# Performance work log

Hardware: AMD Instinct MI355X
Metric: run time of the kernel (lower is better)

Reference implementation:

```python
import jax, jax.numpy as jnp
import numpy as np

B, S, D = 2, 1024, 1024
H, KV, HD = 16, 4, 64
E, F = 8, 3584
EPS = 1e-5
TOP_K = 2


def setup_inputs() -> dict:
    key = jax.random.key(0)
    ks = jax.random.split(key, 12)
    sc = 0.02
    inv_freq = 1.0 / (10000.0 ** (np.arange(0, HD, 2, dtype=np.float32) / HD))
    freqs = np.outer(np.arange(S, dtype=np.float32), inv_freq)
    emb = np.concatenate([freqs, freqs], axis=-1)  # [S, HD]
    return {
        'x': jax.random.normal(ks[0], (B, S, D), jnp.float32),
        'ln1_w': jnp.ones((D,), jnp.float32),
        'ln2_w': jnp.ones((D,), jnp.float32),
        'wq': jax.random.normal(ks[1], (H * HD, D), jnp.float32) * sc,
        'wk': jax.random.normal(ks[2], (KV * HD, D), jnp.float32) * sc,
        'wv': jax.random.normal(ks[3], (KV * HD, D), jnp.float32) * sc,
        'wo': jax.random.normal(ks[4], (D, H * HD), jnp.float32) * sc,
        'gate_w': jax.random.normal(ks[5], (E, D), jnp.float32) * sc,
        'w1': jax.random.normal(ks[6], (E, F, D), jnp.float32) * sc,
        'w2': jax.random.normal(ks[7], (E, D, F), jnp.float32) * sc,
        'w3': jax.random.normal(ks[8], (E, F, D), jnp.float32) * sc,
        'cos': jnp.asarray(np.cos(emb)),
        'sin': jnp.asarray(np.sin(emb)),
    }


def _rms_norm(x, w):
    var = jnp.mean(jnp.square(x), axis=-1, keepdims=True)
    return x * jax.lax.rsqrt(var + EPS) * w


def _rotate_half(x):
    x1, x2 = jnp.split(x, 2, axis=-1)
    return jnp.concatenate([-x2, x1], axis=-1)


def _attn(h, wq, wk, wv, wo, cos, sin):
    # h: [B,S,D]
    q = (h @ wq.T).reshape(B, S, H, HD).transpose(0, 2, 1, 3)      # [B,H,S,HD]
    k = (h @ wk.T).reshape(B, S, KV, HD).transpose(0, 2, 1, 3)     # [B,KV,S,HD]
    v = (h @ wv.T).reshape(B, S, KV, HD).transpose(0, 2, 1, 3)
    c = cos[None, None, :S, :]
    s = sin[None, None, :S, :]
    q = q * c + _rotate_half(q) * s
    k = k * c + _rotate_half(k) * s
    k = jnp.repeat(k, H // KV, axis=1)  # GQA expand -> [B,H,S,HD]
    v = jnp.repeat(v, H // KV, axis=1)
    scores = jnp.einsum('bhqd,bhkd->bhqk', q, k) / jnp.sqrt(jnp.float32(HD))
    causal = jnp.tril(jnp.ones((S, S), bool))
    scores = jnp.where(causal[None, None], scores, jnp.float32(-1e30))
    probs = jax.nn.softmax(scores, axis=-1)
    out = jnp.einsum('bhqk,bhkd->bhqd', probs, v)
    out = out.transpose(0, 2, 1, 3).reshape(B, S, H * HD)
    return out @ wo.T


def _moe(h, gate_w, w1, w2, w3):
    T = B * S
    hs = h.reshape(T, D)
    probs = jax.nn.softmax(hs @ gate_w.T, axis=-1)       # [T,E]
    _, sel = jax.lax.top_k(probs, TOP_K)                  # [T,2]
    rw = jnp.take_along_axis(probs, sel, axis=-1)
    rw = rw / jnp.sum(rw, axis=-1, keepdims=True)
    cw = jnp.zeros((T, E), hs.dtype).at[jnp.arange(T)[:, None], sel].add(rw)  # [T,E] combine weights
    h1 = jnp.einsum('td,efd->tef', hs, w1)               # [T,E,F]
    h3 = jnp.einsum('td,efd->tef', hs, w3)
    inter = jax.nn.silu(h1) * h3
    out = jnp.einsum('tef,edf,te->td', inter, w2, cw)
    return out.reshape(B, S, D)


def reference(x, ln1_w, ln2_w, wq, wk, wv, wo, gate_w, w1, w2, w3, cos, sin):
    h = x + _attn(_rms_norm(x, ln1_w), wq, wk, wv, wo, cos, sin)
    h = h + _moe(_rms_norm(h, ln2_w), gate_w, w1, w2, w3)
    return h
```

## Files before the change

### kernel.cpp

```cpp
#include <hip/hip_runtime.h>

typedef unsigned short u16;
using short8 = __attribute__((ext_vector_type(8))) short;
using f32x4  = __attribute__((ext_vector_type(4))) float;

#define TQ   2048
#define DM   1024
#define SLEN 1024
#define FDIM 3584
#define NEXP 8

static __device__ __forceinline__ u16 f2bf(float f) {
  union { float f; unsigned u; } a; a.f = f;
  unsigned r = a.u + 0x7fffu + ((a.u >> 16) & 1u);
  return (u16)(r >> 16);
}
static __device__ __forceinline__ float bf2f(u16 u) {
  union { unsigned u; float f; } a; a.u = ((unsigned)u) << 16;
  return a.f;
}
static __device__ __forceinline__ unsigned cvtpk(float lo, float hi) {
  unsigned r;
  asm volatile("v_cvt_pk_bf16_f32 %0, %1, %2" : "=v"(r) : "v"(lo), "v"(hi));
  return r;
}

static __device__ __forceinline__ void gload16(const void* g, void* l) {
  __builtin_amdgcn_global_load_lds((const __attribute__((address_space(1))) void*)g,
                                   (__attribute__((address_space(3))) void*)l, 16, 0, 0);
}

static __device__ __forceinline__ int xcd_lid(int bid, int cpx) {
  return (bid & 7) * cpx + (bid >> 3);
}

static __device__ __forceinline__ void cvtwr8(float4 a, float4 b, u16* dst) {
  uint4 u;
  u.x = cvtpk(a.x, a.y); u.y = cvtpk(a.z, a.w);
  u.z = cvtpk(b.x, b.y); u.w = cvtpk(b.z, b.w);
  *(uint4*)dst = u;
}

__global__ __launch_bounds__(256) void fused_pre_kernel(
    const float* __restrict__ x, const float* __restrict__ ln1,
    u16* __restrict__ oh, u16* __restrict__ ol,
    const float* __restrict__ wq, const float* __restrict__ wk,
    const float* __restrict__ wv, const float* __restrict__ wo,
    u16* __restrict__ qkvh, u16* __restrict__ qkvl,
    u16* __restrict__ woh, u16* __restrict__ wol) {
  int tid = threadIdx.x;
  if (blockIdx.x < 2048) {
    int t = blockIdx.x;
    const float4* xr = (const float4*)(x + (size_t)t * DM);
    float4 v = xr[tid];
    float ss = v.x * v.x + v.y * v.y + v.z * v.z + v.w * v.w;
#pragma unroll
    for (int m = 1; m < 64; m <<= 1) ss += __shfl_xor(ss, m);
    __shared__ float red[4];
    if ((tid & 63) == 0) red[tid >> 6] = ss;
    __syncthreads();
    float tot = red[0] + red[1] + red[2] + red[3];
    float sc = rsqrtf(tot * (1.0f / DM) + 1e-5f);
    float4 wv_ = ((const float4*)ln1)[tid];
    float o0 = v.x * sc * wv_.x, o1 = v.y * sc * wv_.y;
    float o2 = v.z * sc * wv_.z, o3 = v.w * sc * wv_.w;
    ushort4 hh;
    hh.x = f2bf(o0); hh.y = f2bf(o1); hh.z = f2bf(o2); hh.w = f2bf(o3);
    *(ushort4*)(oh + (size_t)t * DM + tid * 4) = hh;
    ushort4 ll;
    ll.x = f2bf(o0 - bf2f(hh.x)); ll.y = f2bf(o1 - bf2f(hh.y));
    ll.z = f2bf(o2 - bf2f(hh.z)); ll.w = f2bf(o3 - bf2f(hh.w));
    *(ushort4*)(ol + (size_t)t * DM + tid * 4) = ll;
    return;
  }
  int wb = blockIdx.x - 2048;
  for (int i = wb * 256 + tid; i < 655360; i += 640 * 256) {
    int el = i * 4;
    const float* src; u16 *dh, *dl;
    if (el < 1572864) {
      int r = el >> 10, c = el & 1023;
      if (r < 1024) src = wq + el;
      else if (r < 1280) src = wk + (r - 1024) * 1024 + c;
      else src = wv + (r - 1280) * 1024 + c;
      dh = qkvh + el; dl = qkvl + el;
    } else {
      int e2 = el - 1572864;
      src = wo + e2; dh = woh + e2; dl = wol + e2;
    }
    float4 v = *(const float4*)src;
    ushort4 h, l;
    h.x = f2bf(v.x); h.y = f2bf(v.y); h.z = f2bf(v.z); h.w = f2bf(v.w);
    l.x = f2bf(v.x - bf2f(h.x)); l.y = f2bf(v.y - bf2f(h.y));
    l.z = f2bf(v.z - bf2f(h.z)); l.w = f2bf(v.w - bf2f(h.w));
    *(ushort4*)dh = h; *(ushort4*)dl = l;
  }
}

__global__ __launch_bounds__(256) void rmsnorm_gate_kernel(
    const float* __restrict__ x, const float* __restrict__ w,
    const float* __restrict__ gw, u16* __restrict__ oh,
    int* cnt, int* tok_e, int* tok_pos, float* tok_w) {
  int t = blockIdx.x, tid = threadIdx.x;
  float4 v = ((const float4*)(x + (size_t)t * DM))[tid];
  float ss = v.x * v.x + v.y * v.y + v.z * v.z + v.w * v.w;
#pragma unroll
  for (int m = 1; m < 64; m <<= 1) ss += __shfl_xor(ss, m);
  __shared__ float red[4];
  __shared__ float gred[4][8];
  if ((tid & 63) == 0) red[tid >> 6] = ss;
  __syncthreads();
  float tot = red[0] + red[1] + red[2] + red[3];
  float sc = rsqrtf(tot * (1.0f / DM) + 1e-5f);
  float4 wv_ = ((const float4*)w)[tid];
  float o0 = v.x * sc * wv_.x, o1 = v.y * sc * wv_.y;
  float o2 = v.z * sc * wv_.z, o3 = v.w * sc * wv_.w;
  ushort4 hh;
  hh.x = f2bf(o0); hh.y = f2bf(o1); hh.z = f2bf(o2); hh.w = f2bf(o3);
  *(ushort4*)(oh + (size_t)t * DM + tid * 4) = hh;
  float acc[8];
#pragma unroll
  for (int e = 0; e < 8; e++) {
    float4 ge = ((const float4*)(gw + e * DM))[tid];
    acc[e] = o0 * ge.x + o1 * ge.y + o2 * ge.z + o3 * ge.w;
  }
#pragma unroll
  for (int e = 0; e < 8; e++)
#pragma unroll
    for (int m = 1; m < 64; m <<= 1) acc[e] += __shfl_xor(acc[e], m);
  int lane = tid & 63, wvi = tid >> 6;
  if (lane == 0)
#pragma unroll
    for (int e = 0; e < 8; e++) gred[wvi][e] = acc[e];
  __syncthreads();
  if (tid == 0) {
    float l[8];
#pragma unroll
    for (int e = 0; e < 8; e++)
      l[e] = gred[0][e] + gred[1][e] + gred[2][e] + gred[3][e];
    int i0 = 0;
#pragma unroll
    for (int e = 1; e < 8; e++) if (l[e] > l[i0]) i0 = e;
    int i1 = -1;
#pragma unroll
    for (int e = 0; e < 8; e++) if (e != i0 && (i1 < 0 || l[e] > l[i1])) i1 = e;
    float w0 = 1.0f;
    float w1 = expf(l[i1] - l[i0]);
    float rs = 1.0f / (w0 + w1);
    int p0 = atomicAdd(&cnt[i0], 1);
    int p1 = atomicAdd(&cnt[i1], 1);
    tok_e[t * 2] = i0; tok_e[t * 2 + 1] = i1;
    tok_pos[t * 2] = p0; tok_pos[t * 2 + 1] = p1;
    tok_w[t * 2] = w0 * rs; tok_w[t * 2 + 1] = w1 * rs;
  }
}

__global__ __launch_bounds__(256) void qkv_rope_kernel(
    const u16* __restrict__ Ah, const u16* __restrict__ Al,
    const u16* __restrict__ Wh, const u16* __restrict__ Wl,
    const float* __restrict__ cosT, const float* __restrict__ sinT,
    u16* __restrict__ qh, u16* __restrict__ ql,
    u16* __restrict__ kh, u16* __restrict__ kl,
    u16* __restrict__ vh, u16* __restrict__ vl, int cpx) {
  __shared__ __align__(16) char pool[73728];
  u16 (*sAh)[128][32] = (u16(*)[128][32])pool;
  u16 (*sAl)[128][32] = (u16(*)[128][32])(pool + 24576);
  u16 (*sWh)[64][32]  = (u16(*)[64][32])(pool + 49152);
  u16 (*sWl)[64][32]  = (u16(*)[64][32])(pool + 61440);
  float (*sEpi)[65]   = (float(*)[65])pool;
  int lid = xcd_lid(blockIdx.x, cpx);
  int bm = lid & 15, bn = lid >> 4;
  int tid = threadIdx.x, lane = tid & 63, w = tid >> 6;
  int wm = w >> 1, wn = w & 1;
  int qi = lane & 15, g = lane >> 4;
  int lr = lane >> 2, lc = (lane & 3) * 8;
  const u16* pa0 = Ah + (size_t)(bm * 128 + w * 16 + lr) * DM + lc;
  const u16* pa1 = pa0 + 64 * DM;
  const u16* pl0 = Al + (size_t)(bm * 128 + w * 16 + lr) * DM + lc;
  const u16* pl1 = pl0 + 64 * DM;
  const u16* pw  = Wh + (size_t)(bn * 64 + w * 16 + lr) * DM + lc;
  const u16* pwl = Wl + (size_t)(bn * 64 + w * 16 + lr) * DM + lc;
  f32x4 acc[4][2] = {};
#define STGQ(buf, kk) do { \
    gload16(pa0 + (kk), &sAh[buf][w * 16][0]); \
    gload16(pa1 + (kk), &sAh[buf][64 + w * 16][0]); \
    gload16(pl0 + (kk), &sAl[buf][w * 16][0]); \
    gload16(pl1 + (kk), &sAl[buf][64 + w * 16][0]); \
    gload16(pw  + (kk), &sWh[buf][w * 16][0]); \
    gload16(pwl + (kk), &sWl[buf][w * 16][0]); } while (0)
  STGQ(0, 0);
  STGQ(1, 32);
  for (int ks = 0; ks < 32; ks++) {
    int cur = ks % 3;
    if (ks == 31) asm volatile("s_waitcnt vmcnt(0) lgkmcnt(0)" ::: "memory");
    else          asm volatile("s_waitcnt vmcnt(6) lgkmcnt(0)" ::: "memory");
    __builtin_amdgcn_s_barrier();
    short8 afh[4], afl[4], bfh[2], bfl[2];
#pragma unroll
    for (int i = 0; i < 4; i++) {
      afh[i] = *(short8*)&sAh[cur][wm * 64 + i * 16 + qi][g * 8];
      afl[i] = *(short8*)&sAl[cur][wm * 64 + i * 16 + qi][g * 8];
    }
#pragma unroll
    for (int i = 0; i < 2; i++) {
      bfh[i] = *(short8*)&sWh[cur][wn * 32 + i * 16 + qi][g * 8];
      bfl[i] = *(short8*)&sWl[cur][wn * 32 + i * 16 + qi][g * 8];
    }
    __builtin_amdgcn_s_setprio(1);
#pragma unroll
    for (int mi = 0; mi < 4; mi++)
#pragma unroll
      for (int ni = 0; ni < 2; ni++) {
        f32x4 a = acc[mi][ni];
        a = __builtin_amdgcn_mfma_f32_16x16x32_bf16(afh[mi], bfh[ni], a, 0, 0, 0);
        a = __builtin_amdgcn_mfma_f32_16x16x32_bf16(afl[mi], bfh[ni], a, 0, 0, 0);
        a = __builtin_amdgcn_mfma_f32_16x16x32_bf16(afh[mi], bfl[ni], a, 0, 0, 0);
        acc[mi][ni] = a;
      }
    __builtin_amdgcn_s_setprio(0);
    if (ks < 30) STGQ((ks + 2) % 3, (ks + 2) * 32);
  }
#undef STGQ
  __syncthreads();
#pragma unroll
  for (int mi = 0; mi < 4; mi++)
#pragma unroll
    for (int ni = 0; ni < 2; ni++)
#pragma unroll
      for (int r = 0; r < 4; r++)
        sEpi[wm * 64 + mi * 16 + g * 4 + r][wn * 32 + ni * 16 + qi] = acc[mi][ni][r];
  __syncthreads();
  int r0 = tid >> 1, hc = (tid & 1) * 16;
  int t = bm * 128 + r0;
  int s = t & (SLEN - 1);
  union { ushort u[16]; uint4 v[2]; } h1, l1, h2, l2;
  if (bn < 20) {
#pragma unroll
    for (int j = 0; j < 16; j++) {
      int d = hc + j;
      float c = cosT[s * 64 + d], sn = sinT[s * 64 + d];
      float x1 = sEpi[r0][d], x2 = sEpi[r0][d + 32];
      float o1 = x1 * c - x2 * sn;
      float o2 = x2 * c + x1 * sn;
      h1.u[j] = f2bf(o1); l1.u[j] = f2bf(o1 - bf2f(h1.u[j]));
      h2.u[j] = f2bf(o2); l2.u[j] = f2bf(o2 - bf2f(h2.u[j]));
    }
    u16 *dh, *dl; size_t base;
    if (bn < 16) { dh = qh; dl = ql; base = (size_t)t * DM + bn * 64; }
    else         { dh = kh; dl = kl; base = (size_t)t * 256 + (bn - 16) * 64; }
    *(uint4*)(dh + base + hc)      = h1.v[0];
    *(uint4*)(dh + base + hc + 8)  = h1.v[1];
    *(uint4*)(dh + base + 32 + hc)     = h2.v[0];
    *(uint4*)(dh + base + 32 + hc + 8) = h2.v[1];
    *(uint4*)(dl + base + hc)      = l1.v[0];
    *(uint4*)(dl + base + hc + 8)  = l1.v[1];
    *(uint4*)(dl + base + 32 + hc)     = l2.v[0];
    *(uint4*)(dl + base + 32 + hc + 8) = l2.v[1];
  } else {
#pragma unroll
    for (int j = 0; j < 16; j++) {
      float x1 = sEpi[r0][hc + j], x2 = sEpi[r0][hc + 32 + j];
      h1.u[j] = f2bf(x1); l1.u[j] = f2bf(x1 - bf2f(h1.u[j]));
      h2.u[j] = f2bf(x2); l2.u[j] = f2bf(x2 - bf2f(h2.u[j]));
    }
    size_t base = (size_t)t * 256 + (bn - 20) * 64;
    *(uint4*)(vh + base + hc)      = h1.v[0];
    *(uint4*)(vh + base + hc + 8)  = h1.v[1];
    *(uint4*)(vh + base + 32 + hc)     = h2.v[0];
    *(uint4*)(vh + base + 32 + hc + 8) = h2.v[1];
    *(uint4*)(vl + base + hc)      = l1.v[0];
    *(uint4*)(vl + base + hc + 8)  = l1.v[1];
    *(uint4*)(vl + base + 32 + hc)     = l2.v[0];
    *(uint4*)(vl + base + 32 + hc + 8) = l2.v[1];
  }
}

template <bool RESID>
__global__ __launch_bounds__(256) void gemm_split3_kernel(
    const u16* __restrict__ Ah, const u16* __restrict__ Al,
    const u16* __restrict__ Wh, const u16* __restrict__ Wl,
    float* __restrict__ C, const float* __restrict__ resid, int N, int cpx) {
  __shared__ u16 sAh[3][128][32], sAl[3][128][32], sWh[3][64][32], sWl[3][64][32];
  int lid = xcd_lid(blockIdx.x, cpx);
  int bm = lid & 15, bn = lid >> 4;
  int tid = threadIdx.x, lane = tid & 63, w = tid >> 6;
  int wm = w >> 1, wn = w & 1;
  int qi = lane & 15, g = lane >> 4;
  int lr = lane >> 2, lc = (lane & 3) * 8;
  const u16* pa0 = Ah + (size_t)(bm * 128 + w * 16 + lr) * DM + lc;
  const u16* pa1 = pa0 + 64 * DM;
  const u16* pl0 = Al + (size_t)(bm * 128 + w * 16 + lr) * DM + lc;
  const u16* pl1 = pl0 + 64 * DM;
  const u16* pw  = Wh + (size_t)(bn * 64 + w * 16 + lr) * DM + lc;
  const u16* pwl = Wl + (size_t)(bn * 64 + w * 16 + lr) * DM + lc;
  f32x4 acc[4][2] = {};
#define STG3(buf, kk) do { \
    gload16(pa0 + (kk), &sAh[buf][w * 16][0]); \
    gload16(pa1 + (kk), &sAh[buf][64 + w * 16][0]); \
    gload16(pl0 + (kk), &sAl[buf][w * 16][0]); \
    gload16(pl1 + (kk), &sAl[buf][64 + w * 16][0]); \
    gload16(pw  + (kk), &sWh[buf][w * 16][0]); \
    gload16(pwl + (kk), &sWl[buf][w * 16][0]); } while (0)
  STG3(0, 0);
  STG3(1, 32);
  for (int ks = 0; ks < 32; ks++) {
    int cur = ks % 3;
    if (ks == 31) asm volatile("s_waitcnt vmcnt(0) lgkmcnt(0)" ::: "memory");
    else          asm volatile("s_waitcnt vmcnt(6) lgkmcnt(0)" ::: "memory");
    __builtin_amdgcn_s_barrier();
    short8 afh[4], afl[4], bfh[2], bfl[2];
#pragma unroll
    for (int i = 0; i < 4; i++) {
      afh[i] = *(short8*)&sAh[cur][wm * 64 + i * 16 + qi][g * 8];
      afl[i] = *(short8*)&sAl[cur][wm * 64 + i * 16 + qi][g * 8];
    }
#pragma unroll
    for (int i = 0; i < 2; i++) {
      bfh[i] = *(short8*)&sWh[cur][wn * 32 + i * 16 + qi][g * 8];
      bfl[i] = *(short8*)&sWl[cur][wn * 32 + i * 16 + qi][g * 8];
    }
    __builtin_amdgcn_s_setprio(1);
#pragma unroll
    for (int mi = 0; mi < 4; mi++)
#pragma unroll
      for (int ni = 0; ni < 2; ni++) {
        f32x4 a = acc[mi][ni];
        a = __builtin_amdgcn_mfma_f32_16x16x32_bf16(afh[mi], bfh[ni], a, 0, 0, 0);
        a = __builtin_amdgcn_mfma_f32_16x16x32_bf16(afl[mi], bfh[ni], a, 0, 0, 0);
        a = __builtin_amdgcn_mfma_f32_16x16x32_bf16(afh[mi], bfl[ni], a, 0, 0, 0);
        acc[mi][ni] = a;
      }
    __builtin_amdgcn_s_setprio(0);
    if (ks < 30) STG3((ks + 2) % 3, (ks + 2) * 32);
  }
#undef STG3
#pragma unroll
  for (int mi = 0; mi < 4; mi++)
#pragma unroll
    for (int ni = 0; ni < 2; ni++) {
      int col = bn * 64 + wn * 32 + ni * 16 + qi;
#pragma unroll
      for (int r = 0; r < 4; r++) {
        int row = bm * 128 + wm * 64 + mi * 16 + g * 4 + r;
        float val = acc[mi][ni][r];
        if (RESID) val += resid[(size_t)row * N + col];
        C[(size_t)row * N + col] = val;
      }
    }
}

__global__ __launch_bounds__(256) void attn_kernel(
    const u16* __restrict__ qh, const u16* __restrict__ ql,
    const u16* __restrict__ kh, const u16* __restrict__ kl,
    const u16* __restrict__ vh, const u16* __restrict__ vl,
    u16* __restrict__ oh, u16* __restrict__ ol) {
  __shared__ u16 sKh[64][72], sKl[64][72];
  __shared__ u16 sVh[64][72], sVl[64][72];
  __shared__ u16 sPh[4][16][72], sPl[4][16][72];
  int idx = blockIdx.x & 255;
  int p = idx & 7;
  int bh = idx >> 3;
  int b = bh >> 4, h = bh & 15, kvh = h >> 2;
  int qt = (blockIdx.x < 256) ? p : (15 - p);
  int tid = threadIdx.x, lane = tid & 63, w = tid >> 6;
  int qi = lane & 15, g = lane >> 4;
  int qrow = qt * 64 + w * 16 + qi;
  size_t qbase = ((size_t)(b * SLEN + qrow)) * DM + h * 64;
  short8 qfh[2], qfl[2];
#pragma unroll
  for (int ds = 0; ds < 2; ds++) {
    qfh[ds] = *(const short8*)(qh + qbase + ds * 32 + g * 8);
    qfl[ds] = *(const short8*)(ql + qbase + ds * 32 + g * 8);
  }
  f32x4 oacc[4] = {};
  float mrun = -1e30f, lrun = 0.f;
  int ktiles = qt + 1;
  for (int kt = 0; kt < ktiles; kt++) {
    __syncthreads();
    {
      int r = tid >> 3, cs = (tid & 7) * 8;
#pragma unroll
      for (int rr = 0; rr < 64; rr += 32) {
        int key = kt * 64 + rr + r;
        size_t src = ((size_t)(b * SLEN + key)) * 256 + kvh * 64 + cs;
        *(short8*)&sKh[rr + r][cs] = *(const short8*)(kh + src);
        *(short8*)&sKl[rr + r][cs] = *(const short8*)(kl + src);
        short8 vv = *(const short8*)(vh + src);
        short8 vv2 = *(const short8*)(vl + src);
#pragma unroll
        for (int j = 0; j < 8; j++) {
          sVh[cs + j][rr + r] = (u16)vv[j];
          sVl[cs + j][rr + r] = (u16)vv2[j];
        }
      }
    }
    __syncthreads();
    f32x4 sa[4];
#pragma unroll
    for (int kf = 0; kf < 4; kf++) {
      f32x4 a = {};
#pragma unroll
      for (int ds = 0; ds < 2; ds++) {
        short8 kfh = *(short8*)&sKh[kf * 16 + qi][ds * 32 + g * 8];
        short8 kfl = *(short8*)&sKl[kf * 16 + qi][ds * 32 + g * 8];
        a = __builtin_amdgcn_mfma_f32_16x16x32_bf16(kfh, qfh[ds], a, 0, 0, 0);
        a = __builtin_amdgcn_mfma_f32_16x16x32_bf16(kfl, qfh[ds], a, 0, 0, 0);
        a = __builtin_amdgcn_mfma_f32_16x16x32_bf16(kfh, qfl[ds], a, 0, 0, 0);
      }
      sa[kf] = a;
    }
    int qg = qt * 64 + w * 16 + qi;
    float sv[4][4];
    float tmax = -1e30f;
#pragma unroll
    for (int kf = 0; kf < 4; kf++)
#pragma unroll
      for (int r = 0; r < 4; r++) {
        int key = kt * 64 + kf * 16 + g * 4 + r;
        float s = sa[kf][r] * 0.125f;
        s = (key <= qg) ? s : -1e30f;
        sv[kf][r] = s;
        tmax = fmaxf(tmax, s);
      }
    tmax = fmaxf(tmax, __shfl_xor(tmax, 16));
    tmax = fmaxf(tmax, __shfl_xor(tmax, 32));
    float mn = fmaxf(mrun, tmax);
    float alpha = expf(mrun - mn);
    float psum = 0.f;
#pragma unroll
    for (int kf = 0; kf < 4; kf++) {
      float p0 = expf(sv[kf][0] - mn), p1 = expf(sv[kf][1] - mn);
      float p2 = expf(sv[kf][2] - mn), p3 = expf(sv[kf][3] - mn);
      psum += p0 + p1 + p2 + p3;
      ushort4 ph, pl;
      ph.x = f2bf(p0); ph.y = f2bf(p1); ph.z = f2bf(p2); ph.w = f2bf(p3);
      pl.x = f2bf(p0 - bf2f(ph.x)); pl.y = f2bf(p1 - bf2f(ph.y));
      pl.z = f2bf(p2 - bf2f(ph.z)); pl.w = f2bf(p3 - bf2f(ph.w));
      *(ushort4*)&sPh[w][qi][kf * 16 + g * 4] = ph;
      *(ushort4*)&sPl[w][qi][kf * 16 + g * 4] = pl;
    }
    psum += __shfl_xor(psum, 16);
    psum += __shfl_xor(psum, 32);
    lrun = lrun * alpha + psum;
    mrun = mn;
#pragma unroll
    for (int df = 0; df < 4; df++) {
      oacc[df][0] *= alpha; oacc[df][1] *= alpha;
      oacc[df][2] *= alpha; oacc[df][3] *= alpha;
    }
#pragma unroll
    for (int ks = 0; ks < 2; ks++) {
      short8 pfh = *(short8*)&sPh[w][qi][ks * 32 + g * 8];
      short8 pfl = *(short8*)&sPl[w][qi][ks * 32 + g * 8];
#pragma unroll
      for (int df = 0; df < 4; df++) {
        short8 vfh = *(short8*)&sVh[df * 16 + qi][ks * 32 + g * 8];
        short8 vfl = *(short8*)&sVl[df * 16 + qi][ks * 32 + g * 8];
        f32x4 a = oacc[df];
        a = __builtin_amdgcn_mfma_f32_16x16x32_bf16(vfh, pfh, a, 0, 0, 0);
        a = __builtin_amdgcn_mfma_f32_16x16x32_bf16(vfl, pfh, a, 0, 0, 0);
        a = __builtin_amdgcn_mfma_f32_16x16x32_bf16(vfh, pfl, a, 0, 0, 0);
        oacc[df] = a;
      }
    }
  }
  float inv = 1.0f / lrun;
  size_t obase = ((size_t)(b * SLEN + qt * 64 + w * 16 + qi)) * DM + h * 64;
#pragma unroll
  for (int df = 0; df < 4; df++) {
    float o0 = oacc[df][0] * inv, o1 = oacc[df][1] * inv;
    float o2 = oacc[df][2] * inv, o3 = oacc[df][3] * inv;
    ushort4 hh, ll;
    hh.x = f2bf(o0); hh.y = f2bf(o1); hh.z = f2bf(o2); hh.w = f2bf(o3);
    ll.x = f2bf(o0 - bf2f(hh.x)); ll.y = f2bf(o1 - bf2f(hh.y));
    ll.z = f2bf(o2 - bf2f(hh.z)); ll.w = f2bf(o3 - bf2f(hh.w));
    *(ushort4*)(oh + obase + df * 16 + g * 4) = hh;
    *(ushort4*)(ol + obase + df * 16 + g * 4) = ll;
  }
}

__global__ void zero8_kernel(int* p) { if (threadIdx.x < 8) p[threadIdx.x] = 0; }

__global__ void schedule_kernel(const int* cnt, int* offs, int* mt,
                                int* row_e, int* row_bm) {
  if (threadIdx.x == 0) {
    int s = 0, m = 0;
    for (int e = 0; e < 8; e++) {
      offs[e] = s;
      int nb = (cnt[e] + 127) >> 7;
      for (int i = 0; i < nb; i++) { row_e[m] = e; row_bm[m] = i; m++; }
      s += cnt[e];
    }
    *mt = m;
  }
}

__global__ __launch_bounds__(256) void gather_kernel(
    const u16* __restrict__ hn2b, const int* __restrict__ tok_e,
    const int* __restrict__ tok_pos, const float* __restrict__ tok_w,
    const int* __restrict__ offs, u16* __restrict__ Xg,
    int* __restrict__ pair_tok, int* __restrict__ pair_slot, float* __restrict__ pair_w) {
  int t = blockIdx.x;
#pragma unroll
  for (int slot = 0; slot < 2; slot++) {
    int e = tok_e[t * 2 + slot];
    int p = offs[e] + tok_pos[t * 2 + slot];
    ((ushort4*)(Xg + (size_t)p * DM))[threadIdx.x] =
        ((const ushort4*)(hn2b + (size_t)t * DM))[threadIdx.x];
    if (threadIdx.x == 0) {
      pair_tok[p] = t; pair_slot[p] = slot; pair_w[p] = tok_w[t * 2 + slot];
    }
  }
}

__global__ __launch_bounds__(256) void moe_gemm13_kernel(
    const u16* __restrict__ Xg, const float* __restrict__ w1,
    const float* __restrict__ w3, const int* __restrict__ cnt,
    const int* __restrict__ offs, const int* __restrict__ mt,
    const int* __restrict__ row_e, const int* __restrict__ row_bm,
    u16* __restrict__ inter) {
  __shared__ u16 sA[3][128][32];
  __shared__ u16 sW1[3][64][32], sW3[3][64][32];
  int MT = *mt;
  int active = MT * 56;
  int cpx = (active + 7) >> 3;
  int xg8 = blockIdx.x >> 3;
  if (xg8 >= cpx) return;
  int lid = (blockIdx.x & 7) * cpx + xg8;
  if (lid >= active) return;
  int mrow = lid % MT, bn = lid / MT;
  int e = row_e[mrow], bm = row_bm[mrow];
  int count = cnt[e], off = offs[e];
  const u16* A = Xg + (size_t)off * DM;
  const float* W1 = w1 + (size_t)e * FDIM * DM;
  const float* W3 = w3 + (size_t)e * FDIM * DM;
  int tid = threadIdx.x, lane = tid & 63, w = tid >> 6;
  int wm = w >> 1, wn = w & 1;
  int qi = lane & 15, g = lane >> 4;
  int lrA = lane >> 2, lcA = (lane & 3) * 8;
  int ga0 = bm * 128 + w * 32 + lrA;      if (ga0 >= count) ga0 = count - 1;
  int ga1 = bm * 128 + w * 32 + 16 + lrA; if (ga1 >= count) ga1 = count - 1;
  const u16* pa0 = A + (size_t)ga0 * DM + lcA;
  const u16* pa1 = A + (size_t)ga1 * DM + lcA;
  int r16 = lane >> 2;
  int rW = w * 16 + r16;
  int cW = (lane & 3) * 8;
  const float* q1 = W1 + (size_t)(bn * 64 + rW) * DM + cW;
  const float* q3 = W3 + (size_t)(bn * 64 + rW) * DM + cW;
  int uW = ((lane & 3) ^ (r16 & 3)) * 8;
  f32x4 acc1[4][2] = {}, acc3[4][2] = {};
  float4 p1a = *(const float4*)q1, p1b = *(const float4*)(q1 + 4);
  float4 p3a = *(const float4*)q3, p3b = *(const float4*)(q3 + 4);
  float4 v1a = *(const float4*)(q1 + 32), v1b = *(const float4*)(q1 + 36);
  float4 v3a = *(const float4*)(q3 + 32), v3b = *(const float4*)(q3 + 36);
  __builtin_amdgcn_sched_barrier(0);
  gload16(pa0, &sA[0][w * 32][0]);
  gload16(pa1, &sA[0][w * 32 + 16][0]);
  gload16(pa0 + 32, &sA[1][w * 32][0]);
  gload16(pa1 + 32, &sA[1][w * 32 + 16][0]);
  asm volatile("s_waitcnt vmcnt(8)" ::: "memory");
  cvtwr8(p1a, p1b, &sW1[0][rW][uW]);
  cvtwr8(p3a, p3b, &sW3[0][rW][uW]);
  for (int ks = 0; ks < 32; ks++) {
    int cur = ks % 3;
    if (ks == 0)       asm volatile("s_waitcnt vmcnt(2) lgkmcnt(0)" ::: "memory");
    else if (ks == 31) asm volatile("s_waitcnt vmcnt(0) lgkmcnt(0)" ::: "memory");
    else               asm volatile("s_waitcnt vmcnt(6) lgkmcnt(0)" ::: "memory");
    __builtin_amdgcn_s_barrier();
    short8 af[4], b1[2], b3[2];
#pragma unroll
    for (int i = 0; i < 4; i++)
      af[i] = *(short8*)&sA[cur][wm * 64 + i * 16 + qi][g * 8];
#pragma unroll
    for (int ni = 0; ni < 2; ni++) {
      int rt = wn * 32 + ni * 16 + qi;
      int ui = (g ^ (rt & 3)) * 8;
      b1[ni] = *(short8*)&sW1[cur][rt][ui];
      b3[ni] = *(short8*)&sW3[cur][rt][ui];
    }
    __builtin_amdgcn_s_setprio(1);
#pragma unroll
    for (int mi = 0; mi < 4; mi++)
#pragma unroll
      for (int ni = 0; ni < 2; ni++) {
        acc1[mi][ni] = __builtin_amdgcn_mfma_f32_16x16x32_bf16(af[mi], b1[ni], acc1[mi][ni], 0, 0, 0);
        acc3[mi][ni] = __builtin_amdgcn_mfma_f32_16x16x32_bf16(af[mi], b3[ni], acc3[mi][ni], 0, 0, 0);
      }
    __builtin_amdgcn_s_setprio(0);
    if (ks < 31) {
      int nb = (ks + 1) % 3;
      cvtwr8(v1a, v1b, &sW1[nb][rW][uW]);
      cvtwr8(v3a, v3b, &sW3[nb][rW][uW]);
      if (ks < 30) {
        int k2 = (ks + 2) * 32;
        v1a = *(const float4*)(q1 + k2); v1b = *(const float4*)(q1 + k2 + 4);
        v3a = *(const float4*)(q3 + k2); v3b = *(const float4*)(q3 + k2 + 4);
        __builtin_amdgcn_sched_barrier(0);
        int ab = (ks + 2) % 3;
        gload16(pa0 + k2, &sA[ab][w * 32][0]);
        gload16(pa1 + k2, &sA[ab][w * 32 + 16][0]);
      }
    }
  }
#pragma unroll
  for (int mi = 0; mi < 4; mi++)
#pragma unroll
    for (int r = 0; r < 4; r++) {
      int row = bm * 128 + wm * 64 + mi * 16 + g * 4 + r;
      if (row < count) {
        size_t obase = (size_t)(off + row) * FDIM + bn * 64 + wn * 32;
#pragma unroll
        for (int ni = 0; ni < 2; ni++) {
          float c1 = acc1[mi][ni][r], c3 = acc3[mi][ni][r];
          float sv = c1 / (1.0f + expf(-c1)) * c3;
          inter[obase + ni * 16 + qi] = f2bf(sv);
        }
      }
    }
}

__global__ __launch_bounds__(256) void moe_gemm2_kernel(
    const u16* __restrict__ inter, const float* __restrict__ w2,
    const int* __restrict__ cnt, const int* __restrict__ offs,
    const int* __restrict__ mt, const int* __restrict__ row_e,
    const int* __restrict__ row_bm,
    const int* __restrict__ pair_tok, const int* __restrict__ pair_slot,
    const float* __restrict__ pair_w, float* __restrict__ pout) {
  __shared__ u16 sA[3][128][32];
  __shared__ u16 sW[3][64][32];
  int MT = *mt;
  int active = MT * 16;
  int cpx = (active + 7) >> 3;
  int xg8 = blockIdx.x >> 3;
  if (xg8 >= cpx) return;
  int lid = (blockIdx.x & 7) * cpx + xg8;
  if (lid >= active) return;
  int mrow = lid % MT, bn = lid / MT;
  int e = row_e[mrow], bm = row_bm[mrow];
  int count = cnt[e], off = offs[e];
  const u16* A = inter + (size_t)off * FDIM;
  const float* W = w2 + (size_t)e * DM * FDIM;
  int tid = threadIdx.x, lane = tid & 63, w = tid >> 6;
  int wm = w >> 1, wn = w & 1;
  int qi = lane & 15, g = lane >> 4;
  int lrA = lane >> 2, lcA = (lane & 3) * 8;
  int ga0 = bm * 128 + w * 32 + lrA;      if (ga0 >= count) ga0 = count - 1;
  int ga1 = bm * 128 + w * 32 + 16 + lrA; if (ga1 >= count) ga1 = count - 1;
  const u16* pa0 = A + (size_t)ga0 * FDIM + lcA;
  const u16* pa1 = A + (size_t)ga1 * FDIM + lcA;
  int r16 = lane >> 2;
  int rW = w * 16 + r16;
  int cW = (lane & 3) * 8;
  const float* qw = W + (size_t)(bn * 64 + rW) * FDIM + cW;
  int uW = ((lane & 3) ^ (r16 & 3)) * 8;
  f32x4 acc[4][2] = {};
  const int NK = FDIM / 32;
  float4 ta = *(const float4*)qw, tb = *(const float4*)(qw + 4);
  float4 va = *(const float4*)(qw + 32), vb = *(const float4*)(qw + 36);
  __builtin_amdgcn_sched_barrier(0);
  gload16(pa0, &sA[0][w * 32][0]);
  gload16(pa1, &sA[0][w * 32 + 16][0]);
  gload16(pa0 + 32, &sA[1][w * 32][0]);
  gload16(pa1 + 32, &sA[1][w * 32 + 16][0]);
  asm volatile("s_waitcnt vmcnt(6)" ::: "memory");
  cvtwr8(ta, tb, &sW[0][rW][uW]);
  for (int ks = 0; ks < NK; ks++) {
    int cur = ks % 3;
    if (ks == 0)           asm volatile("s_waitcnt vmcnt(2) lgkmcnt(0)" ::: "memory");
    else if (ks == NK - 1) asm volatile("s_waitcnt vmcnt(0) lgkmcnt(0)" ::: "memory");
    else                   asm volatile("s_waitcnt vmcnt(4) lgkmcnt(0)" ::: "memory");
    __builtin_amdgcn_s_barrier();
    short8 af[4], bfr[2];
#pragma unroll
    for (int i = 0; i < 4; i++)
      af[i] = *(short8*)&sA[cur][wm * 64 + i * 16 + qi][g * 8];
#pragma unroll
    for (int ni = 0; ni < 2; ni++) {
      int rt = wn * 32 + ni * 16 + qi;
      bfr[ni] = *(short8*)&sW[cur][rt][(g ^ (rt & 3)) * 8];
    }
    __builtin_amdgcn_s_setprio(1);
#pragma unroll
    for (int mi = 0; mi < 4; mi++)
#pragma unroll
      for (int ni = 0; ni < 2; ni++)
        acc[mi][ni] = __builtin_amdgcn_mfma_f32_16x16x32_bf16(af[mi], bfr[ni], acc[mi][ni], 0, 0, 0);
    __builtin_amdgcn_s_setprio(0);
    if (ks < NK - 1) {
      int nb = (ks + 1) % 3;
      cvtwr8(va, vb, &sW[nb][rW][uW]);
      if (ks < NK - 2) {
        int k2 = (ks + 2) * 32;
        va = *(const float4*)(qw + k2); vb = *(const float4*)(qw + k2 + 4);
        __builtin_amdgcn_sched_barrier(0);
        int ab = (ks + 2) % 3;
        gload16(pa0 + k2, &sA[ab][w * 32][0]);
        gload16(pa1 + k2, &sA[ab][w * 32 + 16][0]);
      }
    }
  }
#pragma unroll
  for (int mi = 0; mi < 4; mi++)
#pragma unroll
    for (int r = 0; r < 4; r++) {
      int row = bm * 128 + wm * 64 + mi * 16 + g * 4 + r;
      if (row < count) {
        int p = off + row;
        int t = pair_tok[p];
        float wgt = pair_w[p];
        size_t obase = ((size_t)pair_slot[p] * TQ + t) * DM + bn * 64 + wn * 32;
#pragma unroll
        for (int ni = 0; ni < 2; ni++)
          pout[obase + ni * 16 + qi] = acc[mi][ni][r] * wgt;
      }
    }
}

__global__ __launch_bounds__(256) void combine_kernel(
    const float* __restrict__ h, const float* __restrict__ pout, float* __restrict__ out) {
  size_t i = (size_t)blockIdx.x * 256 + threadIdx.x;
  float4 a = ((const float4*)h)[i];
  float4 b0 = ((const float4*)pout)[i];
  float4 b1 = ((const float4*)pout)[i + (size_t)TQ * DM / 4];
  float4 r;
  r.x = a.x + b0.x + b1.x; r.y = a.y + b0.y + b1.y;
  r.z = a.z + b0.z + b1.z; r.w = a.w + b0.w + b1.w;
  ((float4*)out)[i] = r;
}

extern "C" void kernel_launch(void* const* d_in, const int* in_sizes, int n_in,
                              void* d_out, int out_size, void* d_ws, size_t ws_size,
                              hipStream_t stream) {
  (void)in_sizes; (void)n_in; (void)out_size; (void)ws_size;
  const float* x    = (const float*)d_in[0];
  const float* ln1  = (const float*)d_in[1];
  const float* ln2  = (const float*)d_in[2];
  const float* wq   = (const float*)d_in[3];
  const float* wk   = (const float*)d_in[4];
  const float* wv   = (const float*)d_in[5];
  const float* wo   = (const float*)d_in[6];
  const float* gw   = (const float*)d_in[7];
  const float* w1   = (const float*)d_in[8];
  const float* w2   = (const float*)d_in[9];
  const float* w3   = (const float*)d_in[10];
  const float* cosT = (const float*)d_in[11];
  const float* sinT = (const float*)d_in[12];

  char* mb = (char*)d_ws;
  const size_t MB = 1024 * 1024;
  u16*   qhb  = (u16*)(mb + 0 * MB);
  u16*   qlb  = (u16*)(mb + 4 * MB);
  u16*   khb  = (u16*)(mb + 8 * MB);
  u16*   klb  = (u16*)(mb + 9 * MB);
  u16*   vhb  = (u16*)(mb + 10 * MB);
  u16*   vlb  = (u16*)(mb + 11 * MB);
  u16*   hn2b = (u16*)(mb + 0 * MB);
  u16*   ahb  = (u16*)(mb + 12 * MB);
  u16*   alb  = (u16*)(mb + 16 * MB);
  u16*   Xg   = (u16*)(mb + 12 * MB);
  u16*   hn1h = (u16*)(mb + 20 * MB);
  u16*   hn1l = (u16*)(mb + 24 * MB);
  u16*   inter= (u16*)(mb + 20 * MB);
  float* h_res= (float*)(mb + 48 * MB);
  u16*   woh  = (u16*)(mb + 56 * MB);
  u16*   wol  = (u16*)(mb + 58 * MB);
  float* pout = (float*)(mb + 56 * MB);
  u16*   wqkvh= (u16*)(mb + 60 * MB);
  u16*   wqkvl= (u16*)(mb + 63 * MB);
  int*   cnt  = (int*)(mb + 72 * MB);
  int*   offs = cnt + 8;
  int*   mtp  = cnt + 16;
  int*   row_e  = cnt + 17;
  int*   row_bm = cnt + 57;
  int*   tok_e  = cnt + 128;
  int*   tok_pos = tok_e + 4096;
  float* tok_w   = (float*)(tok_pos + 4096);
  int*   pair_tok  = (int*)(tok_w + 4096);
  int*   pair_slot = pair_tok + 4096;
  float* pair_w    = (float*)(pair_slot + 4096);

  fused_pre_kernel<<<2688, 256, 0, stream>>>(x, ln1, hn1h, hn1l,
                                             wq, wk, wv, wo,
                                             wqkvh, wqkvl, woh, wol);
  qkv_rope_kernel<<<384, 256, 0, stream>>>(hn1h, hn1l, wqkvh, wqkvl,
                                           cosT, sinT,
                                           qhb, qlb, khb, klb, vhb, vlb, 48);
  attn_kernel<<<512, 256, 0, stream>>>(qhb, qlb, khb, klb, vhb, vlb, ahb, alb);
  gemm_split3_kernel<true><<<256, 256, 0, stream>>>(ahb, alb, woh, wol, h_res, x, 1024, 32);
  zero8_kernel<<<1, 64, 0, stream>>>(cnt);
  rmsnorm_gate_kernel<<<TQ, 256, 0, stream>>>(h_res, ln2, gw, hn2b,
                                              cnt, tok_e, tok_pos, tok_w);
  schedule_kernel<<<1, 64, 0, stream>>>(cnt, offs, mtp, row_e, row_bm);
  gather_kernel<<<TQ, 256, 0, stream>>>(hn2b, tok_e, tok_pos, tok_w, offs, Xg,
                                        pair_tok, pair_slot, pair_w);
  moe_gemm13_kernel<<<2240, 256, 0, stream>>>(Xg, w1, w3, cnt, offs, mtp,
                                              row_e, row_bm, inter);
  moe_gemm2_kernel<<<640, 256, 0, stream>>>(inter, w2, cnt, offs, mtp,
                                            row_e, row_bm,
                                            pair_tok, pair_slot, pair_w, pout);
  combine_kernel<<<TQ, 256, 0, stream>>>(h_res, pout, (float*)d_out);
}
```

Baseline: 431.1 us.

## Replace token gather copy with indirect row loads in MoE GEMM13

The gather kernel that copied each token's normalized activations into an expert-sorted buffer is removed. The first MoE GEMM now looks up each row's token through pair_tok and loads directly from hn2b, and a small pair_kernel builds only the index and weight arrays. Zeroing of the expert counters is folded into fused_pre_kernel, so zero8_kernel is no longer launched. This removes a roughly 8 MB copy and two launches, at the cost of scattered row reads in the GEMM A-tile loads.

```diff
diff --git a/kernel.cpp b/kernel.cpp
--- a/kernel.cpp
+++ b/kernel.cpp
@@ -47,7 +47,7 @@
     const float* __restrict__ wq, const float* __restrict__ wk,
     const float* __restrict__ wv, const float* __restrict__ wo,
     u16* __restrict__ qkvh, u16* __restrict__ qkvl,
-    u16* __restrict__ woh, u16* __restrict__ wol) {
+    u16* __restrict__ woh, u16* __restrict__ wol, int* __restrict__ cnt) {
   int tid = threadIdx.x;
   if (blockIdx.x < 2048) {
     int t = blockIdx.x;
@@ -74,6 +74,7 @@
     return;
   }
   int wb = blockIdx.x - 2048;
+  if (wb == 0 && tid < 8) cnt[tid] = 0;
   for (int i = wb * 256 + tid; i < 655360; i += 640 * 256) {
     int el = i * 4;
     const float* src; u16 *dh, *dl;
@@ -478,8 +479,6 @@
   }
 }
 
-__global__ void zero8_kernel(int* p) { if (threadIdx.x < 8) p[threadIdx.x] = 0; }
-
 __global__ void schedule_kernel(const int* cnt, int* offs, int* mt,
                                 int* row_e, int* row_bm) {
   if (threadIdx.x == 0) {
@@ -494,26 +493,23 @@
   }
 }
 
-__global__ __launch_bounds__(256) void gather_kernel(
-    const u16* __restrict__ hn2b, const int* __restrict__ tok_e,
-    const int* __restrict__ tok_pos, const float* __restrict__ tok_w,
-    const int* __restrict__ offs, u16* __restrict__ Xg,
-    int* __restrict__ pair_tok, int* __restrict__ pair_slot, float* __restrict__ pair_w) {
-  int t = blockIdx.x;
+__global__ __launch_bounds__(64) void pair_kernel(
+    const int* __restrict__ tok_e, const int* __restrict__ tok_pos,
+    const float* __restrict__ tok_w, const int* __restrict__ offs,
+    int* __restrict__ pair_tok, int* __restrict__ pair_slot,
+    float* __restrict__ pair_w) {
+  int t = blockIdx.x * 64 + threadIdx.x;
 #pragma unroll
   for (int slot = 0; slot < 2; slot++) {
     int e = tok_e[t * 2 + slot];
     int p = offs[e] + tok_pos[t * 2 + slot];
-    ((ushort4*)(Xg + (size_t)p * DM))[threadIdx.x] =
-        ((const ushort4*)(hn2b + (size_t)t * DM))[threadIdx.x];
-    if (threadIdx.x == 0) {
-      pair_tok[p] = t; pair_slot[p] = slot; pair_w[p] = tok_w[t * 2 + slot];
-    }
+    pair_tok[p] = t; pair_slot[p] = slot; pair_w[p] = tok_w[t * 2 + slot];
   }
 }
 
 __global__ __launch_bounds__(256) void moe_gemm13_kernel(
-    const u16* __restrict__ Xg, const float* __restrict__ w1,
+    const u16* __restrict__ hn2b, const int* __restrict__ pair_tok,
+    const float* __restrict__ w1,
     const float* __restrict__ w3, const int* __restrict__ cnt,
     const int* __restrict__ offs, const int* __restrict__ mt,
     const int* __restrict__ row_e, const int* __restrict__ row_bm,
@@ -530,7 +526,6 @@
   int mrow = lid % MT, bn = lid / MT;
   int e = row_e[mrow], bm = row_bm[mrow];
   int count = cnt[e], off = offs[e];
-  const u16* A = Xg + (size_t)off * DM;
   const float* W1 = w1 + (size_t)e * FDIM * DM;
   const float* W3 = w3 + (size_t)e * FDIM * DM;
   int tid = threadIdx.x, lane = tid & 63, w = tid >> 6;
@@ -539,8 +534,10 @@
   int lrA = lane >> 2, lcA = (lane & 3) * 8;
   int ga0 = bm * 128 + w * 32 + lrA;      if (ga0 >= count) ga0 = count - 1;
   int ga1 = bm * 128 + w * 32 + 16 + lrA; if (ga1 >= count) ga1 = count - 1;
-  const u16* pa0 = A + (size_t)ga0 * DM + lcA;
-  const u16* pa1 = A + (size_t)ga1 * DM + lcA;
+  int t0 = pair_tok[off + ga0];
+  int t1 = pair_tok[off + ga1];
+  const u16* pa0 = hn2b + (size_t)t0 * DM + lcA;
+  const u16* pa1 = hn2b + (size_t)t1 * DM + lcA;
   int r16 = lane >> 2;
   int rW = w * 16 + r16;
   int cW = (lane & 3) * 8;
@@ -756,7 +753,6 @@
   u16*   hn2b = (u16*)(mb + 0 * MB);
   u16*   ahb  = (u16*)(mb + 12 * MB);
   u16*   alb  = (u16*)(mb + 16 * MB);
-  u16*   Xg   = (u16*)(mb + 12 * MB);
   u16*   hn1h = (u16*)(mb + 20 * MB);
   u16*   hn1l = (u16*)(mb + 24 * MB);
   u16*   inter= (u16*)(mb + 20 * MB);
@@ -780,19 +776,18 @@
 
   fused_pre_kernel<<<2688, 256, 0, stream>>>(x, ln1, hn1h, hn1l,
                                              wq, wk, wv, wo,
-                                             wqkvh, wqkvl, woh, wol);
+                                             wqkvh, wqkvl, woh, wol, cnt);
   qkv_rope_kernel<<<384, 256, 0, stream>>>(hn1h, hn1l, wqkvh, wqkvl,
                                            cosT, sinT,
                                            qhb, qlb, khb, klb, vhb, vlb, 48);
   attn_kernel<<<512, 256, 0, stream>>>(qhb, qlb, khb, klb, vhb, vlb, ahb, alb);
   gemm_split3_kernel<true><<<256, 256, 0, stream>>>(ahb, alb, woh, wol, h_res, x, 1024, 32);
-  zero8_kernel<<<1, 64, 0, stream>>>(cnt);
   rmsnorm_gate_kernel<<<TQ, 256, 0, stream>>>(h_res, ln2, gw, hn2b,
                                               cnt, tok_e, tok_pos, tok_w);
   schedule_kernel<<<1, 64, 0, stream>>>(cnt, offs, mtp, row_e, row_bm);
-  gather_kernel<<<TQ, 256, 0, stream>>>(hn2b, tok_e, tok_pos, tok_w, offs, Xg,
-                                        pair_tok, pair_slot, pair_w);
-  moe_gemm13_kernel<<<2240, 256, 0, stream>>>(Xg, w1, w3, cnt, offs, mtp,
+  pair_kernel<<<32, 64, 0, stream>>>(tok_e, tok_pos, tok_w, offs,
+                                     pair_tok, pair_slot, pair_w);
+  moe_gemm13_kernel<<<2240, 256, 0, stream>>>(hn2b, pair_tok, w1, w3, cnt, offs, mtp,
                                               row_e, row_bm, inter);
   moe_gemm2_kernel<<<640, 256, 0, stream>>>(inter, w2, cnt, offs, mtp,
                                             row_e, row_bm,
```

New measurement: 427.0 us. Within noise of the previous version (-0.9%).
